# Optimization experiments

Hardware: AMD Instinct MI355X
Metric: run time of the kernel (lower is better)

The kernel has to match this reference:

```python
import jax, jax.numpy as jnp
import numpy as np

N = 50000      # nodes
E = 800000     # edges (avg degree 16)
F_IN = 128
H = 128        # hidden_channels
C = 10         # num_classes
S = 5          # Chebyshev order K
B = 8          # graphs in batch


def setup_inputs() -> dict:
    key = jax.random.key(0)
    ks = jax.random.split(key, 9)
    x = jax.random.normal(ks[0], (N, F_IN), jnp.float32)
    edge_index = jax.random.randint(ks[1], (2, E), 0, N, dtype=jnp.int64)
    batch = jnp.sort(jax.random.randint(ks[2], (N,), 0, B, dtype=jnp.int64))
    lambda_max = 2.0 * jnp.ones((B,), jnp.float32)
    W1 = jax.random.normal(ks[3], (S, F_IN, H), jnp.float32) * 0.05
    b1 = jax.random.normal(ks[4], (H,), jnp.float32) * 0.05
    W2 = jax.random.normal(ks[5], (S, H, H), jnp.float32) * 0.05
    b2 = jax.random.normal(ks[6], (H,), jnp.float32) * 0.05
    Wlin = jax.random.normal(ks[7], (H, C), jnp.float32) * 0.05
    blin = jax.random.normal(ks[8], (C,), jnp.float32) * 0.05
    return {"x": x, "edge_index": edge_index, "batch": batch,
            "lambda_max": lambda_max, "W1": W1, "b1": b1,
            "W2": W2, "b2": b2, "Wlin": Wlin, "blin": blin}


def _cheb_conv(x, row, col, w_edge, diag, W, b):
    # scaled Laplacian matvec: L_hat v = scatter(w_edge * v[col] -> row) + diag * v
    def Lhat(v):
        msg = v[col] * w_edge[:, None]                       # [E, d]
        return jax.ops.segment_sum(msg, row, num_segments=N) + diag[:, None] * v

    Tx0 = x
    out = Tx0 @ W[0]
    Tx1 = Lhat(Tx0)
    out = out + Tx1 @ W[1]
    for k in range(2, W.shape[0]):                           # Chebyshev recurrence
        Tx2 = 2.0 * Lhat(Tx1) - Tx0
        out = out + Tx2 @ W[k]
        Tx0, Tx1 = Tx1, Tx2
    return out + b


def reference(x, edge_index, batch, lambda_max, W1, b1, W2, b2, Wlin, blin):
    row, col = edge_index[0], edge_index[1]
    # sym-normalized Laplacian L = I - D^{-1/2} A D^{-1/2}; L_hat = 2L/lambda_max - I
    deg = jax.ops.segment_sum(jnp.ones((E,), x.dtype), row, num_segments=N)
    dis = jnp.where(deg > 0, jax.lax.rsqrt(jnp.maximum(deg, 1e-12)), 0.0)
    lam_e = lambda_max[batch[row]]                           # per-edge lambda_max
    w_edge = -2.0 * dis[row] * dis[col] / lam_e              # off-diagonal of L_hat
    diag = 2.0 / lambda_max[batch] - 1.0                     # diagonal of L_hat per node

    h = jax.nn.relu(_cheb_conv(x, row, col, w_edge, diag, W1, b1))
    h = jax.nn.relu(_cheb_conv(h, row, col, w_edge, diag, W2, b2))

    # global_mean_pool over batch assignment
    sums = jax.ops.segment_sum(h, batch, num_segments=B)     # [B, H]
    counts = jax.ops.segment_sum(jnp.ones((N, 1), h.dtype), batch, num_segments=B)
    pooled = sums / jnp.maximum(counts, 1.0)
    return pooled @ Wlin + blin                              # [B, C] logits (softmax unused in forward)
```

## Files before the change

### kernel.cpp

```cpp
#include <hip/hip_runtime.h>
#include <hip/hip_bf16.h>
#include <stdint.h>

typedef __attribute__((ext_vector_type(8))) short bf16x8;
typedef __attribute__((ext_vector_type(4))) float f32x4;

__device__ __forceinline__ float bf16lo_to_f(uint32_t u) { return __uint_as_float(u << 16); }
__device__ __forceinline__ float bf16hi_to_f(uint32_t u) { return __uint_as_float(u & 0xffff0000u); }
__device__ __forceinline__ uint16_t f_to_bf16(float f) {
    uint32_t u = __float_as_uint(f);
    uint32_t r = u + 0x7fff + ((u >> 16) & 1);
    return (uint16_t)(r >> 16);
}


__global__ void k_deg(const int* __restrict__ row, int* __restrict__ deg, int E) {
    int e = blockIdx.x * blockDim.x + threadIdx.x;
    if (e < E) atomicAdd(&deg[row[e]], 1);
}

__global__ void k_psum(const int* __restrict__ deg, int* __restrict__ psum, int N) {
    __shared__ int sh[256];
    int t = threadIdx.x;
    int idx = blockIdx.x * 256 + t;
    sh[t] = idx < N ? ((deg[idx] + 7) & ~7) : 0;
    __syncthreads();
    for (int o = 128; o > 0; o >>= 1) {
        if (t < o) sh[t] += sh[t + o];
        __syncthreads();
    }
    if (t == 0) psum[blockIdx.x] = sh[0];
}

__global__ void k_scanp(const int* __restrict__ psum, int* __restrict__ poff,
                        int* __restrict__ offs, int nb, int N) {
    __shared__ int sh[256];
    int t = threadIdx.x;
    int per = (nb + 255) >> 8;
    int base = t * per;
    int s = 0;
    for (int i = 0; i < per; i++) { int idx = base + i; if (idx < nb) s += psum[idx]; }
    sh[t] = s;
    __syncthreads();
    for (int o = 1; o < 256; o <<= 1) {
        int u = (t >= o) ? sh[t - o] : 0;
        __syncthreads();
        sh[t] += u;
        __syncthreads();
    }
    int run = sh[t] - s;
    for (int i = 0; i < per; i++) {
        int idx = base + i;
        if (idx < nb) { poff[idx] = run; run += psum[idx]; }
    }
    if (t == 255) offs[N] = sh[255];
}

__global__ void k_offs(const int* __restrict__ deg, const int* __restrict__ poff,
                       int* __restrict__ offs, int* __restrict__ cursor,
                       const int* __restrict__ batch, const float* __restrict__ lam,
                       float* __restrict__ dis, float* __restrict__ diag, int N) {
    __shared__ int sh[256];
    int t = threadIdx.x;
    int idx = blockIdx.x * 256 + t;
    int d = idx < N ? deg[idx] : 0;
    int v = (d + 7) & ~7;
    sh[t] = v;
    __syncthreads();
    for (int o = 1; o < 256; o <<= 1) {
        int u = (t >= o) ? sh[t - o] : 0;
        __syncthreads();
        sh[t] += u;
        __syncthreads();
    }
    if (idx < N) {
        int ex = poff[blockIdx.x] + sh[t] - v;
        offs[idx] = ex;
        cursor[idx] = ex;
        dis[idx] = d > 0 ? rsqrtf((float)d) : 0.f;
        diag[idx] = 2.f / lam[batch[idx]] - 1.f;
    }
}

__global__ void k_csr(const int* __restrict__ row, const int* __restrict__ col,
                      int* __restrict__ cursor, uint16_t* __restrict__ csr, int E) {
    int e = blockIdx.x * blockDim.x + threadIdx.x;
    if (e < E) {
        int r = row[e];
        int pos = atomicAdd(&cursor[r], 1);
        __builtin_nontemporal_store((uint16_t)col[e], &csr[pos]);
    }
}

__global__ void k_prepw(const float* __restrict__ W1, uint16_t* __restrict__ Wt1,
                        const float* __restrict__ W2, uint16_t* __restrict__ Wt2) {
    int i = blockIdx.x * blockDim.x + threadIdx.x;
    const float* W = W1; uint16_t* Wt = Wt1;
    if (i >= 128 * 640) { i -= 128 * 640; W = W2; Wt = Wt2; }
    int o = i / 640, kk = i % 640;
    Wt[(size_t)o * 640 + kk] = f_to_bf16(W[(size_t)kk * 128 + o]);
}

__global__ void __launch_bounds__(256) k_castx(const float* __restrict__ x,
        uint16_t* __restrict__ Txb, int8_t* __restrict__ Txq,
        const float* __restrict__ dis, float* __restrict__ mS, int N) {
    int n = (blockIdx.x * blockDim.x + threadIdx.x) >> 6;
    int lane = threadIdx.x & 63;
    if (n >= N) return;
    float2 v = ((const float2*)x)[(size_t)n * 64 + lane];
    uint32_t p = (uint32_t)f_to_bf16(v.x) | ((uint32_t)f_to_bf16(v.y) << 16);
    ((uint32_t*)Txb)[(size_t)n * 320 + lane] = p;
    float m = fmaxf(fabsf(v.x), fabsf(v.y));
    for (int o = 1; o < 64; o <<= 1) m = fmaxf(m, __shfl_xor(m, o));
    float inv = m > 0.f ? 127.f / m : 0.f;
    int qx = (int)rintf(v.x * inv), qy = (int)rintf(v.y * inv);
    uint16_t qp = (uint16_t)((qx & 0xff) | ((qy & 0xff) << 8));
    *(uint16_t*)(Txq + (size_t)n * 640 + 2 * lane) = qp;
    if (lane == 0) mS[n] = (m > 0.f ? m * (1.f / 127.f) : 0.f) * dis[n];
}

__global__ void __launch_bounds__(256) k_lhat(
        int8_t* __restrict__ Txq, uint16_t* __restrict__ Txb,
        const int* __restrict__ offs, const uint16_t* __restrict__ csr,
        const float* __restrict__ diag, const float* __restrict__ dis,
        float* __restrict__ mS, int N,
        int src, int dst, int prev, float alpha, int use_prev) {
    int n = (blockIdx.x * blockDim.x + threadIdx.x) >> 6;
    int lane = threadIdx.x & 63;
    if (n >= N) return;
    int beg = offs[n], end = offs[n + 1];
    float dgn = diag[n], dn = dis[n];
    float aS = -alpha * dn * (dgn + 1.0f);
    const float* mSrc = mS + (size_t)src * (N + 1);
    const int8_t* qbase = Txq + src * 128 + 2 * lane;
    float ax = 0.f, ay = 0.f;
    for (int e = beg; e < end; e += 8) {
        uint4 cw = *(const uint4*)(csr + e);
        int cc[8] = { (int)(cw.x & 0xffff), (int)(cw.x >> 16),
                      (int)(cw.y & 0xffff), (int)(cw.y >> 16),
                      (int)(cw.z & 0xffff), (int)(cw.z >> 16),
                      (int)(cw.w & 0xffff), (int)(cw.w >> 16) };
        float mm[8];
        uint16_t qv[8];
#pragma unroll
        for (int u = 0; u < 8; u++) mm[u] = mSrc[cc[u]];
#pragma unroll
        for (int u = 0; u < 8; u++)
            qv[u] = *(const uint16_t*)(qbase + (size_t)cc[u] * 640);
#pragma unroll
        for (int u = 0; u < 8; u++) {
            float f = aS * mm[u];
            ax = fmaf(f, (float)(int)(int8_t)(qv[u] & 0xff), ax);
            ay = fmaf(f, (float)(int)(int8_t)(qv[u] >> 8), ay);
        }
    }
    const uint32_t* bb = (const uint32_t*)Txb;
    uint32_t sv = bb[(size_t)n * 320 + src * 64 + lane];
    float ad = alpha * dgn;
    ax += ad * bf16lo_to_f(sv);
    ay += ad * bf16hi_to_f(sv);
    if (use_prev) {
        uint32_t pv = bb[(size_t)n * 320 + prev * 64 + lane];
        ax -= bf16lo_to_f(pv);
        ay -= bf16hi_to_f(pv);
    }
    uint32_t outv = (uint32_t)f_to_bf16(ax) | ((uint32_t)f_to_bf16(ay) << 16);
    ((uint32_t*)Txb)[(size_t)n * 320 + dst * 64 + lane] = outv;
    float m = fmaxf(fabsf(ax), fabsf(ay));
    for (int o = 1; o < 64; o <<= 1) m = fmaxf(m, __shfl_xor(m, o));
    float inv = m > 0.f ? 127.f / m : 0.f;
    int qx = (int)rintf(ax * inv), qy = (int)rintf(ay * inv);
    uint16_t qp = (uint16_t)((qx & 0xff) | ((qy & 0xff) << 8));
    *(uint16_t*)(Txq + (size_t)n * 640 + dst * 128 + 2 * lane) = qp;
    if (lane == 0)
        mS[(size_t)dst * (N + 1) + n] = (m > 0.f ? m * (1.f / 127.f) : 0.f) * dn;
}

#define BM 128
#define BK 64
#define LDT 72
#define LDC 132

__global__ void __launch_bounds__(256) k_gemm(
        const uint16_t* __restrict__ A, int lda,
        const uint16_t* __restrict__ Bt,
        const float* __restrict__ bias,
        uint16_t* __restrict__ out, int ldo,
        uint16_t* __restrict__ out2b,
        int8_t* __restrict__ out2q,
        const float* __restrict__ dis, float* __restrict__ mS,
        int M, int Kdim) {
    __shared__ uint16_t smem[BM * LDT + 128 * LDT];
    uint16_t* As = smem;
    uint16_t* Bs = smem + BM * LDT;
    uint16_t* Ct = smem;
    int t = threadIdx.x;
    int w = t >> 6, lane = t & 63;
    int row0 = blockIdx.x * BM;
    int mrow = (w >> 1) * 64, ncol = (w & 1) * 64;

    int ar[4], akc[4];
#pragma unroll
    for (int rep = 0; rep < 4; rep++) {
        int d = rep * 256 + t;
        ar[rep] = d >> 3; akc[rep] = d & 7;
    }

    f32x4 acc[4][4];
#pragma unroll
    for (int i = 0; i < 4; i++)
#pragma unroll
        for (int j = 0; j < 4; j++) acc[i][j] = (f32x4){0.f, 0.f, 0.f, 0.f};

    bf16x8 pa[4], pb[4];
#pragma unroll
    for (int rep = 0; rep < 4; rep++) {
        int grow = row0 + ar[rep];
        bf16x8 va = {0, 0, 0, 0, 0, 0, 0, 0};
        if (grow < M) va = *(const bf16x8*)(A + (size_t)grow * lda + akc[rep] * 8);
        pa[rep] = va;
        pb[rep] = *(const bf16x8*)(Bt + (size_t)ar[rep] * Kdim + akc[rep] * 8);
    }

    for (int k0 = 0; k0 < Kdim; k0 += BK) {
#pragma unroll
        for (int rep = 0; rep < 4; rep++) {
            *(bf16x8*)(&As[ar[rep] * LDT + akc[rep] * 8]) = pa[rep];
            *(bf16x8*)(&Bs[ar[rep] * LDT + akc[rep] * 8]) = pb[rep];
        }
        __syncthreads();
        int kn = k0 + BK;
        if (kn < Kdim) {
#pragma unroll
            for (int rep = 0; rep < 4; rep++) {
                int grow = row0 + ar[rep];
                bf16x8 va = {0, 0, 0, 0, 0, 0, 0, 0};
                if (grow < M) va = *(const bf16x8*)(A + (size_t)grow * lda + kn + akc[rep] * 8);
                pa[rep] = va;
                pb[rep] = *(const bf16x8*)(Bt + (size_t)ar[rep] * Kdim + kn + akc[rep] * 8);
            }
        }
#pragma unroll
        for (int ks = 0; ks < BK; ks += 32) {
            bf16x8 af[4], bfr[4];
#pragma unroll
            for (int i = 0; i < 4; i++) {
                int r = mrow + i * 16 + (lane & 15);
                af[i] = *(const bf16x8*)(&As[r * LDT + ks + (lane >> 4) * 8]);
            }
#pragma unroll
            for (int j = 0; j < 4; j++) {
                int c = ncol + j * 16 + (lane & 15);
                bfr[j] = *(const bf16x8*)(&Bs[c * LDT + ks + (lane >> 4) * 8]);
            }
#pragma unroll
            for (int i = 0; i < 4; i++)
#pragma unroll
                for (int j = 0; j < 4; j++)
                    acc[i][j] = __builtin_amdgcn_mfma_f32_16x16x32_bf16(af[i], bfr[j], acc[i][j], 0, 0, 0);
        }
        __syncthreads();
    }

#pragma unroll
    for (int j = 0; j < 4; j++) {
        int c = ncol + j * 16 + (lane & 15);
        float bv = bias[c];
#pragma unroll
        for (int i = 0; i < 4; i++) {
            int rloc = mrow + i * 16 + (lane >> 4) * 4;
#pragma unroll
            for (int r = 0; r < 4; r++) {
                float v = acc[i][j][r] + bv;
                v = v > 0.f ? v : 0.f;
                Ct[(rloc + r) * LDC + c] = f_to_bf16(v);
            }
        }
    }
    __syncthreads();
#pragma unroll
    for (int rep = 0; rep < 8; rep++) {
        int d = rep * 256 + t;
        int r = d >> 4, c8 = (d & 15) * 8;
        int grow = row0 + r;
        if (grow < M) {
            bf16x8 v = *(const bf16x8*)(&Ct[r * LDC + c8]);
            *(bf16x8*)(out + (size_t)grow * ldo + c8) = v;
            if (out2b) *(bf16x8*)(out2b + (size_t)grow * 640 + c8) = v;
        }
    }
    if (out2q) {
        int r = t >> 1, half = t & 1;
        int grow = row0 + r;
        const uint32_t* crow = (const uint32_t*)0;
        float vmax = 0.f;
        for (int j = 0; j < 32; j++) {
            uint32_t u = *(const uint32_t*)(&Ct[r * LDC + half * 64 + j * 2]);
            vmax = fmaxf(vmax, fmaxf(fabsf(bf16lo_to_f(u)), fabsf(bf16hi_to_f(u))));
        }
        vmax = fmaxf(vmax, __shfl_xor(vmax, 1));
        if (grow < M) {
            float inv = vmax > 0.f ? 127.f / vmax : 0.f;
            for (int j0 = 0; j0 < 16; j0++) {
                uint32_t u0 = *(const uint32_t*)(&Ct[r * LDC + half * 64 + j0 * 4]);
                uint32_t u1 = *(const uint32_t*)(&Ct[r * LDC + half * 64 + j0 * 4 + 2]);
                int q0 = (int)rintf(bf16lo_to_f(u0) * inv);
                int q1 = (int)rintf(bf16hi_to_f(u0) * inv);
                int q2 = (int)rintf(bf16lo_to_f(u1) * inv);
                int q3 = (int)rintf(bf16hi_to_f(u1) * inv);
                uint32_t pk = (q0 & 0xff) | ((q1 & 0xff) << 8) |
                              ((q2 & 0xff) << 16) | ((uint32_t)(q3 & 0xff) << 24);
                *(uint32_t*)(out2q + (size_t)grow * 640 + half * 64 + j0 * 4) = pk;
            }
            if (half == 0)
                mS[grow] = (vmax > 0.f ? vmax * (1.f / 127.f) : 0.f) * dis[grow];
        }
        (void)crow;
    }
}

__global__ void __launch_bounds__(128) k_pool(const uint16_t* __restrict__ h,
        const int* __restrict__ batch, float* __restrict__ pooled, int N, int CH) {
    int f = threadIdx.x;
    int n0 = blockIdx.x * CH;
    if (n0 >= N) return;
    int n1 = min(n0 + CH, N);
    float acc = 0.f;
    int cur = batch[n0];
    for (int n = n0; n < n1; ++n) {
        int b = batch[n];
        if (b != cur) { atomicAdd(&pooled[cur * 128 + f], acc); acc = 0.f; cur = b; }
        acc += __uint_as_float(((uint32_t)h[(size_t)n * 128 + f]) << 16);
    }
    atomicAdd(&pooled[cur * 128 + f], acc);
}

__global__ void k_final(const float* __restrict__ pooled, const int* __restrict__ batch,
                        const float* __restrict__ Wlin, const float* __restrict__ blin,
                        float* __restrict__ out, int N, int B_, int C_) {
    __shared__ int cnt[64];
    int t = threadIdx.x;
    if (t < B_) {
        auto lb = [&](int v) {
            int lo = 0, hi = N;
            while (lo < hi) {
                int mid = (lo + hi) >> 1;
                if (batch[mid] < v) lo = mid + 1; else hi = mid;
            }
            return lo;
        };
        cnt[t] = lb(t + 1) - lb(t);
    }
    __syncthreads();
    if (t < B_ * C_) {
        int b = t / C_, c = t % C_;
        float inv = 1.f / fmaxf((float)cnt[b], 1.f);
        float acc = blin[c];
        for (int f = 0; f < 128; ++f) acc += pooled[b * 128 + f] * inv * Wlin[f * C_ + c];
        out[t] = acc;
    }
}

extern "C" void kernel_launch(void* const* d_in, const int* in_sizes, int n_in,
                              void* d_out, int out_size, void* d_ws, size_t ws_size,
                              hipStream_t stream) {
    const float* x    = (const float*)d_in[0];
    const int*   edge = (const int*)d_in[1];
    const int*   batch= (const int*)d_in[2];
    const float* lam  = (const float*)d_in[3];
    const float* W1   = (const float*)d_in[4];
    const float* b1   = (const float*)d_in[5];
    const float* W2   = (const float*)d_in[6];
    const float* b2   = (const float*)d_in[7];
    const float* Wlin = (const float*)d_in[8];
    const float* blin = (const float*)d_in[9];
    const int E  = in_sizes[1] / 2;
    const int N  = in_sizes[2];
    const int B_ = in_sizes[3];
    const int* row = edge;
    const int* col = edge + E;

    char* ws = (char*)d_ws;
    size_t off = 0;
    auto take = [&](size_t bytes) -> char* {
        char* p = ws + off;
        off = (off + bytes + 255) & ~(size_t)255;
        return p;
    };
    uint16_t* Txb    = (uint16_t*)take((size_t)N * 640 * 2);
    int8_t*   Txq    = (int8_t*)take((size_t)(N + 1) * 640);
    uint16_t* h      = (uint16_t*)take((size_t)N * 128 * 2);
    uint16_t* csr    = (uint16_t*)take(((size_t)E + 8 * (size_t)N) * 2);
    float*    mS     = (float*)take((size_t)5 * (N + 1) * 4);
    int*      deg    = (int*)take((size_t)N * 4);
    int*      offs   = (int*)take((size_t)(N + 1) * 4);
    int*      cursor = (int*)take((size_t)N * 4);
    float*    dis    = (float*)take((size_t)N * 4);
    float*    diag   = (float*)take((size_t)N * 4);
    uint16_t* Wt1    = (uint16_t*)take((size_t)128 * 640 * 2);
    uint16_t* Wt2    = (uint16_t*)take((size_t)128 * 640 * 2);
    float*    pooled = (float*)take((size_t)B_ * 128 * 4);
    const int nb = (N + 255) / 256;
    int*      psum   = (int*)take((size_t)nb * 4);
    int*      poff   = (int*)take((size_t)nb * 4);

    hipMemsetAsync(deg, 0, (size_t)N * 4, stream);
    hipMemsetAsync(pooled, 0, (size_t)B_ * 128 * 4, stream);
    hipMemsetAsync(mS, 0, (size_t)5 * (N + 1) * 4, stream);
    hipMemsetD16Async((hipDeviceptr_t)csr, (unsigned short)N,
                      (size_t)E + 8 * (size_t)N, stream);

    k_deg<<<(E + 255) / 256, 256, 0, stream>>>(row, deg, E);
    k_psum<<<nb, 256, 0, stream>>>(deg, psum, N);
    k_scanp<<<1, 256, 0, stream>>>(psum, poff, offs, nb, N);
    k_offs<<<nb, 256, 0, stream>>>(deg, poff, offs, cursor, batch, lam, dis, diag, N);
    k_csr<<<(E + 255) / 256, 256, 0, stream>>>(row, col, cursor, csr, E);
    k_prepw<<<(2 * 128 * 640) / 256, 256, 0, stream>>>(W1, Wt1, W2, Wt2);
    k_castx<<<(N + 3) / 4, 256, 0, stream>>>(x, Txb, Txq, dis, mS, N);

    const int lblocks = (N + 3) / 4;
    const int gblocks = (N + BM - 1) / BM;

    k_lhat<<<lblocks, 256, 0, stream>>>(Txq, Txb, offs, csr, diag, dis, mS, N, 0, 1, 0, 1.f, 0);
    k_lhat<<<lblocks, 256, 0, stream>>>(Txq, Txb, offs, csr, diag, dis, mS, N, 1, 2, 0, 2.f, 1);
    k_lhat<<<lblocks, 256, 0, stream>>>(Txq, Txb, offs, csr, diag, dis, mS, N, 2, 3, 1, 2.f, 1);
    k_lhat<<<lblocks, 256, 0, stream>>>(Txq, Txb, offs, csr, diag, dis, mS, N, 3, 4, 2, 2.f, 1);
    k_gemm<<<gblocks, 256, 0, stream>>>(Txb, 640, Wt1, b1, h, 128, Txb, Txq, dis, mS, N, 640);

    k_lhat<<<lblocks, 256, 0, stream>>>(Txq, Txb, offs, csr, diag, dis, mS, N, 0, 1, 0, 1.f, 0);
    k_lhat<<<lblocks, 256, 0, stream>>>(Txq, Txb, offs, csr, diag, dis, mS, N, 1, 2, 0, 2.f, 1);
    k_lhat<<<lblocks, 256, 0, stream>>>(Txq, Txb, offs, csr, diag, dis, mS, N, 2, 3, 1, 2.f, 1);
    k_lhat<<<lblocks, 256, 0, stream>>>(Txq, Txb, offs, csr, diag, dis, mS, N, 3, 4, 2, 2.f, 1);
    k_gemm<<<gblocks, 256, 0, stream>>>(Txb, 640, Wt2, b2, h, 128,
                                        (uint16_t*)nullptr, (int8_t*)nullptr, dis, mS, N, 640);

    k_pool<<<(N + 127) / 128, 128, 0, stream>>>(h, batch, pooled, N, 128);
    k_final<<<1, 128, 0, stream>>>(pooled, batch, Wlin, blin, (float*)d_out, N, B_, 10);
}
```

Before: 553.3 us.

## Build CSR via two-level bucket sort with shared-memory atomics

Replaces the global-atomic degree count and CSR scatter with a bucketed approach. Edges are first binned by row>>8 into 256-node buckets using a histogram, a scan and a staged local sort. Then one block per bucket computes degrees and scatters columns into CSR using shared-memory atomics. This is meant to cut contended global atomics and random scattered writes, at the cost of extra kernel launches and an additional 4-byte-per-edge intermediate buffer.

```diff
diff --git a/kernel.cpp b/kernel.cpp
--- a/kernel.cpp
+++ b/kernel.cpp
@@ -14,9 +14,92 @@
 }
 
 
-__global__ void k_deg(const int* __restrict__ row, int* __restrict__ deg, int E) {
-    int e = blockIdx.x * blockDim.x + threadIdx.x;
-    if (e < E) atomicAdd(&deg[row[e]], 1);
+#define BINCH 4096
+
+__global__ void __launch_bounds__(256) k_bhist(const int* __restrict__ row,
+                                               int* __restrict__ bhist, int E) {
+    __shared__ int sh[256];
+    int t = threadIdx.x;
+    sh[t] = 0;
+    __syncthreads();
+    int stride = gridDim.x * blockDim.x;
+    for (int e = blockIdx.x * blockDim.x + t; e < E; e += stride)
+        atomicAdd(&sh[row[e] >> 8], 1);
+    __syncthreads();
+    if (sh[t]) atomicAdd(&bhist[t], sh[t]);
+}
+
+__global__ void k_bscan(const int* __restrict__ bhist, int* __restrict__ gbase,
+                        int* __restrict__ gcur, int nbk) {
+    __shared__ int sh[256];
+    int t = threadIdx.x;
+    int v = t < nbk ? bhist[t] : 0;
+    sh[t] = v;
+    __syncthreads();
+    for (int o = 1; o < 256; o <<= 1) {
+        int u = (t >= o) ? sh[t - o] : 0;
+        __syncthreads();
+        sh[t] += u;
+        __syncthreads();
+    }
+    gbase[t] = sh[t] - v;
+    gcur[t] = sh[t] - v;
+    if (t == 255) gbase[256] = sh[255];
+}
+
+__global__ void __launch_bounds__(256) k_bin(const int* __restrict__ row,
+        const int* __restrict__ col, int* __restrict__ gcur,
+        uint32_t* __restrict__ bout, int E) {
+    __shared__ uint32_t stage[BINCH];
+    __shared__ int hist[256], hscan[256], hcur[256], gofs[256];
+    int t = threadIdx.x;
+    int e0 = blockIdx.x * BINCH;
+    int ecnt = min(BINCH, E - e0);
+    hist[t] = 0;
+    __syncthreads();
+    for (int i = t; i < ecnt; i += 256)
+        atomicAdd(&hist[row[e0 + i] >> 8], 1);
+    __syncthreads();
+    int v = hist[t];
+    hscan[t] = v;
+    __syncthreads();
+    for (int o = 1; o < 256; o <<= 1) {
+        int u = (t >= o) ? hscan[t - o] : 0;
+        __syncthreads();
+        hscan[t] += u;
+        __syncthreads();
+    }
+    hcur[t] = hscan[t] - v;
+    __syncthreads();
+    for (int i = t; i < ecnt; i += 256) {
+        int r = row[e0 + i];
+        int p = atomicAdd(&hcur[r >> 8], 1);
+        stage[p] = (uint32_t)(r & 255) | ((uint32_t)col[e0 + i] << 8);
+    }
+    __syncthreads();
+    if (v > 0) gofs[t] = atomicAdd(&gcur[t], v);
+    __syncthreads();
+    for (int i = t; i < ecnt; i += 256) {
+        int lo = 0, hi = 255;
+        while (lo < hi) { int mid = (lo + hi) >> 1; if (hscan[mid] > i) hi = mid; else lo = mid + 1; }
+        int b = lo;
+        int local = i - (hscan[b] - hist[b]);
+        bout[gofs[b] + local] = stage[i];
+    }
+}
+
+__global__ void __launch_bounds__(256) k_deg2(const uint32_t* __restrict__ bout,
+        const int* __restrict__ gbase, int* __restrict__ deg, int N) {
+    __shared__ int cnt[256];
+    int t = threadIdx.x, b = blockIdx.x;
+    cnt[t] = 0;
+    __syncthreads();
+    int s = gbase[b], epos = gbase[b + 1];
+    for (int i = s + t; i < epos; i += 256)
+        atomicAdd(&cnt[bout[i] & 255], 1);
+    __syncthreads();
+    int n = b * 256 + t;
+    if (n < N) deg[n] = cnt[t];
 }
 
 __global__ void k_psum(const int* __restrict__ deg, int* __restrict__ psum, int N) {
@@ -57,7 +140,7 @@
 }
 
 __global__ void k_offs(const int* __restrict__ deg, const int* __restrict__ poff,
-                       int* __restrict__ offs, int* __restrict__ cursor,
+                       int* __restrict__ offs,
                        const int* __restrict__ batch, const float* __restrict__ lam,
                        float* __restrict__ dis, float* __restrict__ diag, int N) {
     __shared__ int sh[256];
@@ -74,21 +157,25 @@
         __syncthreads();
     }
     if (idx < N) {
-        int ex = poff[blockIdx.x] + sh[t] - v;
-        offs[idx] = ex;
-        cursor[idx] = ex;
+        offs[idx] = poff[blockIdx.x] + sh[t] - v;
         dis[idx] = d > 0 ? rsqrtf((float)d) : 0.f;
         diag[idx] = 2.f / lam[batch[idx]] - 1.f;
     }
 }
 
-__global__ void k_csr(const int* __restrict__ row, const int* __restrict__ col,
-                      int* __restrict__ cursor, uint16_t* __restrict__ csr, int E) {
-    int e = blockIdx.x * blockDim.x + threadIdx.x;
-    if (e < E) {
-        int r = row[e];
-        int pos = atomicAdd(&cursor[r], 1);
-        __builtin_nontemporal_store((uint16_t)col[e], &csr[pos]);
+__global__ void __launch_bounds__(256) k_csr2(const uint32_t* __restrict__ bout,
+        const int* __restrict__ gbase, const int* __restrict__ offs,
+        uint16_t* __restrict__ csr, int N) {
+    __shared__ int cur[256];
+    int t = threadIdx.x, b = blockIdx.x;
+    int n = b * 256 + t;
+    cur[t] = n < N ? offs[n] : 0;
+    __syncthreads();
+    int s = gbase[b], epos = gbase[b + 1];
+    for (int i = s + t; i < epos; i += 256) {
+        uint32_t v = bout[i];
+        int p = atomicAdd(&cur[v & 255], 1);
+        csr[p] = (uint16_t)(v >> 8);
     }
 }
 
@@ -292,7 +379,6 @@
     if (out2q) {
         int r = t >> 1, half = t & 1;
         int grow = row0 + r;
-        const uint32_t* crow = (const uint32_t*)0;
         float vmax = 0.f;
         for (int j = 0; j < 32; j++) {
             uint32_t u = *(const uint32_t*)(&Ct[r * LDC + half * 64 + j * 2]);
@@ -315,7 +401,6 @@
             if (half == 0)
                 mS[grow] = (vmax > 0.f ? vmax * (1.f / 127.f) : 0.f) * dis[grow];
         }
-        (void)crow;
     }
 }
 
@@ -391,30 +476,36 @@
     int8_t*   Txq    = (int8_t*)take((size_t)(N + 1) * 640);
     uint16_t* h      = (uint16_t*)take((size_t)N * 128 * 2);
     uint16_t* csr    = (uint16_t*)take(((size_t)E + 8 * (size_t)N) * 2);
+    uint32_t* bout   = (uint32_t*)take((size_t)E * 4);
     float*    mS     = (float*)take((size_t)5 * (N + 1) * 4);
     int*      deg    = (int*)take((size_t)N * 4);
     int*      offs   = (int*)take((size_t)(N + 1) * 4);
-    int*      cursor = (int*)take((size_t)N * 4);
     float*    dis    = (float*)take((size_t)N * 4);
     float*    diag   = (float*)take((size_t)N * 4);
     uint16_t* Wt1    = (uint16_t*)take((size_t)128 * 640 * 2);
     uint16_t* Wt2    = (uint16_t*)take((size_t)128 * 640 * 2);
     float*    pooled = (float*)take((size_t)B_ * 128 * 4);
+    int*      bhist  = (int*)take(257 * 4);
+    int*      gbase  = (int*)take(257 * 4);
+    int*      gcur   = (int*)take(257 * 4);
     const int nb = (N + 255) / 256;
     int*      psum   = (int*)take((size_t)nb * 4);
     int*      poff   = (int*)take((size_t)nb * 4);
 
-    hipMemsetAsync(deg, 0, (size_t)N * 4, stream);
     hipMemsetAsync(pooled, 0, (size_t)B_ * 128 * 4, stream);
     hipMemsetAsync(mS, 0, (size_t)5 * (N + 1) * 4, stream);
+    hipMemsetAsync(bhist, 0, 257 * 4, stream);
     hipMemsetD16Async((hipDeviceptr_t)csr, (unsigned short)N,
                       (size_t)E + 8 * (size_t)N, stream);
 
-    k_deg<<<(E + 255) / 256, 256, 0, stream>>>(row, deg, E);
+    k_bhist<<<112, 256, 0, stream>>>(row, bhist, E);
+    k_bscan<<<1, 256, 0, stream>>>(bhist, gbase, gcur, nb);
+    k_bin<<<(E + BINCH - 1) / BINCH, 256, 0, stream>>>(row, col, gcur, bout, E);
+    k_deg2<<<nb, 256, 0, stream>>>(bout, gbase, deg, N);
     k_psum<<<nb, 256, 0, stream>>>(deg, psum, N);
     k_scanp<<<1, 256, 0, stream>>>(psum, poff, offs, nb, N);
-    k_offs<<<nb, 256, 0, stream>>>(deg, poff, offs, cursor, batch, lam, dis, diag, N);
-    k_csr<<<(E + 255) / 256, 256, 0, stream>>>(row, col, cursor, csr, E);
+    k_offs<<<nb, 256, 0, stream>>>(deg, poff, offs, batch, lam, dis, diag, N);
+    k_csr2<<<nb, 256, 0, stream>>>(bout, gbase, offs, csr, N);
     k_prepw<<<(2 * 128 * 640) / 256, 256, 0, stream>>>(W1, Wt1, W2, Wt2);
     k_castx<<<(N + 3) / 4, 256, 0, stream>>>(x, Txb, Txq, dis, mS, N);
 
```

Measured after the change: 513.7 us. -7.2%, faster.
